# Kernel optimization log

Measured on AMD Instinct MI355X. Metric: run time of the kernel, lower is better.

Reference implementation:

```python
import jax, jax.numpy as jnp
import numpy as np

HEADS = 12
DIM_HEAD = 64
WINDOW = 16
SHIFT = 1  # fixed stand-in for random.randint(0, window-1)
SCALE = DIM_HEAD ** -0.5


def window_cls_mask(n, window, shift):
    # Shifted block-diagonal mask over the n-1 non-CLS tokens, CLS attends/attended everywhere.
    size = n - 1
    idx = jnp.arange(size)
    cur = (idx - shift) % window
    left = jnp.clip(idx - cur, 0, size)
    right = jnp.clip(idx + (window - cur), 0, size)
    i = idx[:, None]  # query position
    wmask = (i >= left[None, :]) & (i < right[None, :])  # [size, size]
    full = jnp.ones((n, n), dtype=bool)
    full = full.at[1:, 1:].set(wmask)
    return full  # [n, n] bool


def setup_inputs() -> dict:
    key = jax.random.key(0)
    k1, k2, k3 = jax.random.split(key, 3)
    b, n, dim = 2, 2049, 768
    inner = HEADS * DIM_HEAD
    return {
        "x": jax.random.normal(k1, (b, n, dim), dtype=jnp.float32),
        "w_qkv": jax.random.normal(k2, (dim, 3 * inner), dtype=jnp.float32) * 0.02,
        "w_out": jax.random.normal(k3, (inner, dim), dtype=jnp.float32) * 0.02,
        "b_out": jnp.zeros((dim,), dtype=jnp.float32),
    }


def reference(x, w_qkv, w_out, b_out):
    b, n, dim = x.shape
    h, d = HEADS, DIM_HEAD
    qkv = x @ w_qkv  # [b, n, 3*h*d]
    q, k, v = jnp.split(qkv, 3, axis=-1)
    # b n (h d) -> b h n d
    reshape = lambda t: t.reshape(b, n, h, d).transpose(0, 2, 1, 3)
    q, k, v = reshape(q), reshape(k), reshape(v)
    dots = jnp.einsum('bhid,bhjd->bhij', q, k) * SCALE  # [b, h, n, n]
    mask = window_cls_mask(n, WINDOW, SHIFT)  # [n, n]
    neg = -jnp.finfo(dots.dtype).max
    dots = jnp.where(mask[None, None], dots, neg)
    attn = jax.nn.softmax(dots, axis=-1)
    out = jnp.einsum('bhij,bhjd->bhid', attn, v)  # [b, h, n, d]
    out = out.transpose(0, 2, 1, 3).reshape(b, n, h * d)
    return out @ w_out + b_out
```

## Files before the change

kernel.cpp:

```cpp
#include <hip/hip_runtime.h>
#include <hip/hip_bf16.h>
#include <math.h>

typedef __attribute__((ext_vector_type(8))) __bf16 bf16x8;
typedef __attribute__((ext_vector_type(4))) float f32x4;

#define HEADS 12
#define DHEAD 64
#define NTOK 2049
#define BATCH 2
#define DIM 768
#define QKV3 2304
#define MROWS 4098
#define MP 4224
#define ATT_SCALE 0.125f
#define BKS 64
#define NSPLIT 33
#define PSTRIDE 68

__global__ __launch_bounds__(256) void cvt_x_kernel(const float* __restrict__ x,
                                                    __bf16* __restrict__ xb) {
  int t = blockIdx.x * 256 + threadIdx.x;
  long e = (long)t * 8;
  int row = (int)(e / DIM);
  bf16x8 v;
  if (row < MROWS) {
    const float4 a = *(const float4*)(x + e);
    const float4 b = *(const float4*)(x + e + 4);
    v[0] = (__bf16)a.x; v[1] = (__bf16)a.y; v[2] = (__bf16)a.z; v[3] = (__bf16)a.w;
    v[4] = (__bf16)b.x; v[5] = (__bf16)b.y; v[6] = (__bf16)b.z; v[7] = (__bf16)b.w;
  } else {
#pragma unroll
    for (int j = 0; j < 8; ++j) v[j] = (__bf16)0.f;
  }
  *(bf16x8*)(xb + e) = v;
}

__global__ __launch_bounds__(256) void transpose_cvt_kernel(const float* __restrict__ in,
                                                            __bf16* __restrict__ out,
                                                            int R, int C) {
  __shared__ float tile[32][33];
  int c0 = blockIdx.x * 32, r0 = blockIdx.y * 32;
  int tx = threadIdx.x & 31, ty = threadIdx.x >> 5;
#pragma unroll
  for (int i = 0; i < 4; ++i) {
    int r = ty + i * 8;
    tile[r][tx] = in[(size_t)(r0 + r) * C + c0 + tx];
  }
  __syncthreads();
#pragma unroll
  for (int i = 0; i < 4; ++i) {
    int r = ty + i * 8;
    out[(size_t)(c0 + r) * R + r0 + tx] = (__bf16)tile[tx][r];
  }
}

template <bool BF16_OUT>
__global__ __launch_bounds__(256) void gemm128_kernel(const __bf16* __restrict__ A,
                                                      const __bf16* __restrict__ Bt,
                                                      void* __restrict__ Cv,
                                                      const float* __restrict__ bias,
                                                      int N, int K, int Mvalid) {
  __shared__ __bf16 sA[128 * BKS];
  __shared__ __bf16 sB[128 * BKS];
  const int tid = threadIdx.x;
  const int w = tid >> 6, lane = tid & 63;
  const int m0 = blockIdx.y * 128, n0 = blockIdx.x * 128;
  const int wr = w >> 1, wc = w & 1;
  f32x4 acc[4][4] = {};

  const int srow = (w << 5) + (lane >> 3);
  const int scol = (lane & 7) << 3;

  for (int kt = 0; kt < K; kt += BKS) {
#pragma unroll
    for (int it = 0; it < 4; ++it) {
      int row = srow + (it << 3);
      const __bf16* ga = A + (size_t)(m0 + row) * K + kt + scol;
      const __bf16* gb = Bt + (size_t)(n0 + row) * K + kt + scol;
      int ldsoff = ((w << 2) + it) << 9;
      __builtin_amdgcn_global_load_lds((const __attribute__((address_space(1))) void*)ga,
                                       (__attribute__((address_space(3))) void*)(sA + ldsoff),
                                       16, 0, 0);
      __builtin_amdgcn_global_load_lds((const __attribute__((address_space(1))) void*)gb,
                                       (__attribute__((address_space(3))) void*)(sB + ldsoff),
                                       16, 0, 0);
    }
    __syncthreads();
#pragma unroll
    for (int kk = 0; kk < BKS; kk += 32) {
      bf16x8 af[4], bfr[4];
#pragma unroll
      for (int m = 0; m < 4; ++m)
        af[m] = *(const bf16x8*)&sA[(wr * 64 + m * 16 + (lane & 15)) * BKS + kk + (lane >> 4) * 8];
#pragma unroll
      for (int n = 0; n < 4; ++n)
        bfr[n] = *(const bf16x8*)&sB[(wc * 64 + n * 16 + (lane & 15)) * BKS + kk + (lane >> 4) * 8];
#pragma unroll
      for (int m = 0; m < 4; ++m)
#pragma unroll
        for (int n = 0; n < 4; ++n)
          acc[m][n] = __builtin_amdgcn_mfma_f32_16x16x32_bf16(af[m], bfr[n], acc[m][n], 0, 0, 0);
    }
    __syncthreads();
  }

#pragma unroll
  for (int m = 0; m < 4; ++m) {
#pragma unroll
    for (int n = 0; n < 4; ++n) {
      int col = n0 + wc * 64 + n * 16 + (lane & 15);
      int rbase = m0 + wr * 64 + m * 16 + ((lane >> 4) << 2);
#pragma unroll
      for (int r = 0; r < 4; ++r) {
        int row = rbase + r;
        float val = acc[m][n][r];
        if constexpr (BF16_OUT) {
          ((__bf16*)Cv)[(size_t)row * N + col] = (__bf16)val;
        } else {
          if (row < Mvalid) ((float*)Cv)[(size_t)row * N + col] = val + bias[col];
        }
      }
    }
  }
}

__global__ __launch_bounds__(64) void attn_win_kernel(const __bf16* __restrict__ qkv,
                                                      __bf16* __restrict__ attnb) {
  int bidx = blockIdx.x;
  int hg = bidx % 3; bidx /= 3;
  int blk = bidx % 129;
  int bb = bidx / 129;
  int lane = threadIdx.x;
  int h = hg * 4 + (lane >> 4);
  int qi = lane & 15;
  int t0 = (blk == 0) ? 1 : 2 + 16 * (blk - 1);
  int nt = (blk == 0) ? 1 : ((NTOK - t0) < 16 ? (NTOK - t0) : 16);
  bool active = qi < nt;
  int qt = t0 + (active ? qi : nt - 1);
  const size_t base = (size_t)bb * NTOK * QKV3;

  float q[64];
  {
    const __bf16* qp = qkv + base + (size_t)qt * QKV3 + h * DHEAD;
#pragma unroll
    for (int d0 = 0; d0 < 64; d0 += 8) {
      bf16x8 v = *(const bf16x8*)(qp + d0);
#pragma unroll
      for (int j = 0; j < 8; ++j) q[d0 + j] = (float)v[j];
    }
  }

  float s[17];
  float mx = -3.4e38f;
#pragma unroll
  for (int j = 0; j < 17; ++j) {
    int jc = (j - 1) < (nt - 1) ? (j - 1) : (nt - 1);
    int kt = (j == 0) ? 0 : t0 + jc;
    const __bf16* kp = qkv + base + (size_t)kt * QKV3 + DIM + h * DHEAD;
    float dot = 0.f;
#pragma unroll
    for (int d0 = 0; d0 < 64; d0 += 8) {
      bf16x8 v = *(const bf16x8*)(kp + d0);
#pragma unroll
      for (int jj = 0; jj < 8; ++jj) dot = fmaf(q[d0 + jj], (float)v[jj], dot);
    }
    s[j] = (j <= nt) ? dot * ATT_SCALE : -3.4e38f;
    mx = fmaxf(mx, s[j]);
  }
  float sum = 0.f;
#pragma unroll
  for (int j = 0; j < 17; ++j) {
    s[j] = expf(s[j] - mx);
    sum += s[j];
  }
  float inv = 1.f / sum;

  float o[64];
#pragma unroll
  for (int d = 0; d < 64; ++d) o[d] = 0.f;
#pragma unroll
  for (int j = 0; j < 17; ++j) {
    int jc = (j - 1) < (nt - 1) ? (j - 1) : (nt - 1);
    int vt = (j == 0) ? 0 : t0 + jc;
    const __bf16* vp = qkv + base + (size_t)vt * QKV3 + 2 * DIM + h * DHEAD;
    float p = s[j];
#pragma unroll
    for (int d0 = 0; d0 < 64; d0 += 8) {
      bf16x8 v = *(const bf16x8*)(vp + d0);
#pragma unroll
      for (int jj = 0; jj < 8; ++jj) o[d0 + jj] = fmaf(p, (float)v[jj], o[d0 + jj]);
    }
  }

  if (active) {
    __bf16* op = attnb + (size_t)(bb * NTOK + qt) * DIM + h * DHEAD;
#pragma unroll
    for (int d0 = 0; d0 < 64; d0 += 8) {
      bf16x8 v;
#pragma unroll
      for (int j = 0; j < 8; ++j) v[j] = (__bf16)(o[d0 + j] * inv);
      *(bf16x8*)(op + d0) = v;
    }
  }
}

__global__ __launch_bounds__(64) void attn_cls_part(const __bf16* __restrict__ qkv,
                                                    float* __restrict__ part) {
  int bid = blockIdx.x;
  const int sp = bid % NSPLIT;
  const int bh = bid / NSPLIT;
  const int h = bh % HEADS;
  const int bb = bh / HEADS;
  const int lane = threadIdx.x;
  const size_t base = (size_t)bb * NTOK * QKV3;

  float q[64];
  {
    const __bf16* qp = qkv + base + h * DHEAD;
#pragma unroll
    for (int d0 = 0; d0 < 64; d0 += 8) {
      bf16x8 v = *(const bf16x8*)(qp + d0);
#pragma unroll
      for (int j = 0; j < 8; ++j) q[d0 + j] = (float)v[j];
    }
  }

  const int t = sp * 64 + lane;
  const bool valid = t < NTOK;
  const int tc = valid ? t : NTOK - 1;
  float dot = 0.f;
  {
    const __bf16* kp = qkv + base + (size_t)tc * QKV3 + DIM + h * DHEAD;
#pragma unroll
    for (int d0 = 0; d0 < 64; d0 += 8) {
      bf16x8 v = *(const bf16x8*)(kp + d0);
#pragma unroll
      for (int j = 0; j < 8; ++j) dot = fmaf(q[d0 + j], (float)v[j], dot);
    }
  }
  float s = valid ? dot * ATT_SCALE : -3.4e38f;

  float m = s;
#pragma unroll
  for (int off = 32; off > 0; off >>= 1) m = fmaxf(m, __shfl_xor(m, off, 64));
  float p = valid ? expf(s - m) : 0.f;
  float l = p;
#pragma unroll
  for (int off = 32; off > 0; off >>= 1) l += __shfl_xor(l, off, 64);

  __shared__ float sp_lds[64];
  sp_lds[lane] = p;
  __syncthreads();

  const int nt = (NTOK - sp * 64) < 64 ? (NTOK - sp * 64) : 64;
  float o = 0.f;
  const __bf16* vcol = qkv + base + (size_t)(sp * 64) * QKV3 + 2 * DIM + h * DHEAD + lane;
  for (int tt = 0; tt < nt; ++tt) {
    o = fmaf(sp_lds[tt], (float)vcol[(size_t)tt * QKV3], o);
  }

  float* pb = part + ((size_t)bh * NSPLIT + sp) * PSTRIDE;
  pb[lane] = o;
  if (lane == 0) { pb[64] = m; pb[65] = l; }
}

__global__ __launch_bounds__(64) void attn_cls_reduce(const float* __restrict__ part,
                                                      __bf16* __restrict__ attnb) {
  const int bh = blockIdx.x;
  const int h = bh % HEADS;
  const int bb = bh / HEADS;
  const int lane = threadIdx.x;
  const float* pb0 = part + (size_t)bh * NSPLIT * PSTRIDE;
  float M = -3.4e38f;
#pragma unroll
  for (int i = 0; i < NSPLIT; ++i) M = fmaxf(M, pb0[i * PSTRIDE + 64]);
  float L = 0.f, o = 0.f;
#pragma unroll
  for (int i = 0; i < NSPLIT; ++i) {
    float w = expf(pb0[i * PSTRIDE + 64] - M);
    L = fmaf(pb0[i * PSTRIDE + 65], w, L);
    o = fmaf(pb0[i * PSTRIDE + lane], w, o);
  }
  attnb[(size_t)(bb * NTOK) * DIM + h * DHEAD + lane] = (__bf16)(o / L);
}

extern "C" void kernel_launch(void* const* d_in, const int* in_sizes, int n_in,
                              void* d_out, int out_size, void* d_ws, size_t ws_size,
                              hipStream_t stream) {
  const float* x = (const float*)d_in[0];
  const float* w_qkv = (const float*)d_in[1];
  const float* w_out = (const float*)d_in[2];
  const float* b_out = (const float*)d_in[3];
  float* out = (float*)d_out;

  char* ws = (char*)d_ws;
  __bf16* xb    = (__bf16*)(ws);
  __bf16* wqkvT = (__bf16*)(ws + 6488064);
  __bf16* woutT = (__bf16*)(ws + 6488064 + 3538944);
  __bf16* qkvb  = (__bf16*)(ws + 6488064 + 3538944 + 1179648);
  __bf16* attnb = (__bf16*)(ws + 6488064 + 3538944 + 1179648 + 19464192);
  float*  clsp  = (float*)(ws + 6488064 + 3538944 + 1179648 + 19464192 + 6488064);

  cvt_x_kernel<<<1584, 256, 0, stream>>>(x, xb);
  transpose_cvt_kernel<<<dim3(QKV3 / 32, DIM / 32), 256, 0, stream>>>(w_qkv, wqkvT, DIM, QKV3);
  transpose_cvt_kernel<<<dim3(DIM / 32, DIM / 32), 256, 0, stream>>>(w_out, woutT, DIM, DIM);

  gemm128_kernel<true><<<dim3(QKV3 / 128, MP / 128), 256, 0, stream>>>(
      xb, wqkvT, (void*)qkvb, nullptr, QKV3, DIM, MP);

  attn_win_kernel<<<BATCH * 129 * 3, 64, 0, stream>>>(qkvb, attnb);
  attn_cls_part<<<BATCH * HEADS * NSPLIT, 64, 0, stream>>>(qkvb, clsp);
  attn_cls_reduce<<<BATCH * HEADS, 64, 0, stream>>>(clsp, attnb);

  gemm128_kernel<false><<<dim3(DIM / 128, MP / 128), 256, 0, stream>>>(
      attnb, woutT, (void*)out, b_out, DIM, DIM, MROWS);
}
```

Measured before the change: 175.4 us.

## Double-buffer LDS tiles in bf16 GEMM to overlap global loads with MFMA

The GEMM main loop now uses two LDS buffers for the A and B tiles. It issues the global_load_lds prefetch for the next K tile before running the MFMAs on the current one, with a single barrier per iteration. This is meant to hide global memory latency behind compute in the QKV and output projections. In exchange it doubles LDS use per block to 64KB, which may cut occupancy.

```diff
diff --git a/kernel.cpp b/kernel.cpp
--- a/kernel.cpp
+++ b/kernel.cpp
@@ -61,8 +61,8 @@
                                                       void* __restrict__ Cv,
                                                       const float* __restrict__ bias,
                                                       int N, int K, int Mvalid) {
-  __shared__ __bf16 sA[128 * BKS];
-  __shared__ __bf16 sB[128 * BKS];
+  __shared__ __bf16 sA[2][128 * BKS];
+  __shared__ __bf16 sB[2][128 * BKS];
   const int tid = threadIdx.x;
   const int w = tid >> 6, lane = tid & 63;
   const int m0 = blockIdx.y * 128, n0 = blockIdx.x * 128;
@@ -71,31 +71,42 @@
 
   const int srow = (w << 5) + (lane >> 3);
   const int scol = (lane & 7) << 3;
-
-  for (int kt = 0; kt < K; kt += BKS) {
-#pragma unroll
-    for (int it = 0; it < 4; ++it) {
-      int row = srow + (it << 3);
-      const __bf16* ga = A + (size_t)(m0 + row) * K + kt + scol;
-      const __bf16* gb = Bt + (size_t)(n0 + row) * K + kt + scol;
-      int ldsoff = ((w << 2) + it) << 9;
-      __builtin_amdgcn_global_load_lds((const __attribute__((address_space(1))) void*)ga,
-                                       (__attribute__((address_space(3))) void*)(sA + ldsoff),
-                                       16, 0, 0);
-      __builtin_amdgcn_global_load_lds((const __attribute__((address_space(1))) void*)gb,
-                                       (__attribute__((address_space(3))) void*)(sB + ldsoff),
-                                       16, 0, 0);
-    }
-    __syncthreads();
+  const __bf16* gA = A + (size_t)(m0 + srow) * K + scol;
+  const __bf16* gB = Bt + (size_t)(n0 + srow) * K + scol;
+  const int ldsoff0 = (w << 2) << 9;
+
+  const int nk = K / BKS;
+
+#define STAGE(buf, kt)                                                                   \
+  do {                                                                                   \
+    _Pragma("unroll")                                                                    \
+    for (int it = 0; it < 4; ++it) {                                                     \
+      __builtin_amdgcn_global_load_lds(                                                  \
+          (const __attribute__((address_space(1))) void*)(gA + (size_t)(it * 8) * K + (kt)), \
+          (__attribute__((address_space(3))) void*)(&sA[buf][ldsoff0 + (it << 9)]), 16, 0, 0); \
+      __builtin_amdgcn_global_load_lds(                                                  \
+          (const __attribute__((address_space(1))) void*)(gB + (size_t)(it * 8) * K + (kt)), \
+          (__attribute__((address_space(3))) void*)(&sB[buf][ldsoff0 + (it << 9)]), 16, 0, 0); \
+    }                                                                                    \
+  } while (0)
+
+  STAGE(0, 0);
+  __syncthreads();
+
+  for (int t = 0; t < nk; ++t) {
+    const int cur = t & 1;
+    if (t + 1 < nk) STAGE(cur ^ 1, (t + 1) * BKS);
+    const __bf16* bufA = sA[cur];
+    const __bf16* bufB = sB[cur];
 #pragma unroll
     for (int kk = 0; kk < BKS; kk += 32) {
       bf16x8 af[4], bfr[4];
 #pragma unroll
       for (int m = 0; m < 4; ++m)
-        af[m] = *(const bf16x8*)&sA[(wr * 64 + m * 16 + (lane & 15)) * BKS + kk + (lane >> 4) * 8];
+        af[m] = *(const bf16x8*)&bufA[(wr * 64 + m * 16 + (lane & 15)) * BKS + kk + (lane >> 4) * 8];
 #pragma unroll
       for (int n = 0; n < 4; ++n)
-        bfr[n] = *(const bf16x8*)&sB[(wc * 64 + n * 16 + (lane & 15)) * BKS + kk + (lane >> 4) * 8];
+        bfr[n] = *(const bf16x8*)&bufB[(wc * 64 + n * 16 + (lane & 15)) * BKS + kk + (lane >> 4) * 8];
 #pragma unroll
       for (int m = 0; m < 4; ++m)
 #pragma unroll
@@ -104,6 +115,7 @@
     }
     __syncthreads();
   }
+#undef STAGE
 
 #pragma unroll
   for (int m = 0; m < 4; ++m) {
```

Measured after the change: 174.2 us. Within noise of the previous version (-0.7%).
